# Kernel tuning notes

Hardware: AMD Instinct MI355X
Metric: run time of the kernel (lower is better)

## Reference

```python
import jax, jax.numpy as jnp
import numpy as np

B, L, D = 2, 2048, 1024
NH, KVH, DH = 16, 8, 64
GROUPS = NH // KVH
ROPE_THETA = 10000.0
SPARSITY = 0.5


def setup_inputs() -> dict:
    key = jax.random.key(0)
    ks = jax.random.split(key, 5)
    hidden_states = jax.random.normal(ks[0], (B, L, D), dtype=jnp.float32)
    wq = jax.random.normal(ks[1], (D, NH * DH), dtype=jnp.float32) * 0.02
    wk = jax.random.normal(ks[2], (D, KVH * DH), dtype=jnp.float32) * 0.02
    wv = jax.random.normal(ks[3], (D, KVH * DH), dtype=jnp.float32) * 0.02
    wo = jax.random.normal(ks[4], (NH * DH, D), dtype=jnp.float32) * 0.02
    position_ids = jnp.broadcast_to(jnp.arange(L, dtype=jnp.int64 if jax.config.jax_enable_x64 else jnp.int32), (B, L))
    return {"hidden_states": hidden_states, "wq": wq, "wk": wk, "wv": wv, "wo": wo,
            "position_ids": position_ids}


def _rope_cos_sin(position_ids, dh, theta):
    inv_freq = 1.0 / (theta ** (jnp.arange(0, dh, 2, dtype=jnp.float32) / dh))  # [dh/2]
    freqs = position_ids.astype(jnp.float32)[..., None] * inv_freq              # [B,L,dh/2]
    emb = jnp.concatenate([freqs, freqs], axis=-1)                              # [B,L,dh]
    return jnp.cos(emb)[:, None], jnp.sin(emb)[:, None]                         # [B,1,L,dh]


def _rotate_half(x):
    h = x.shape[-1] // 2
    return jnp.concatenate([-x[..., h:], x[..., :h]], axis=-1)


def _attention(hidden_states, wq, wk, wv, wo, position_ids):
    b, l, _ = hidden_states.shape
    q = (hidden_states @ wq).reshape(b, l, NH, DH).transpose(0, 2, 1, 3)    # [B,NH,L,DH]
    k = (hidden_states @ wk).reshape(b, l, KVH, DH).transpose(0, 2, 1, 3)   # [B,KVH,L,DH]
    v = (hidden_states @ wv).reshape(b, l, KVH, DH).transpose(0, 2, 1, 3)

    cos, sin = _rope_cos_sin(position_ids, DH, ROPE_THETA)
    q = q * cos + _rotate_half(q) * sin
    k = k * cos + _rotate_half(k) * sin

    # repeat_kv: expand kv heads to match query heads (interleaved like torch)
    k = jnp.repeat(k, GROUPS, axis=1)
    v = jnp.repeat(v, GROUPS, axis=1)

    scale = DH ** -0.5
    scores = jnp.einsum("bhqd,bhkd->bhqk", q, k) * scale                    # [B,NH,L,L]

    # dynamic sparsity: keep exactly top_k entries per row (scatter mask, like torch)
    top_k = max(1, int(SPARSITY * l))
    flat = scores.reshape(-1, l)                                            # [N,L]
    _, idx = jax.lax.top_k(flat, top_k)                                     # [N,k]
    rows = jnp.arange(flat.shape[0])[:, None]
    mask = jnp.zeros(flat.shape, dtype=bool).at[rows, idx].set(True)
    min_val = jnp.finfo(flat.dtype).min
    sparse = jnp.where(mask, flat, min_val).reshape(scores.shape)

    probs = jax.nn.softmax(sparse.astype(jnp.float32), axis=-1).astype(q.dtype)
    out = jnp.einsum("bhqk,bhkd->bhqd", probs, v)                            # [B,NH,L,DH]
    out = out.transpose(0, 2, 1, 3).reshape(b, l, NH * DH)
    return out @ wo


def reference(hidden_states, wq, wk, wv, wo, position_ids):
    return _attention(hidden_states, wq, wk, wv, wo, position_ids)
```

## Files before the change

kernel.cpp:

```cpp
#include <hip/hip_runtime.h>
#include <cstdint>
#include <cstddef>

typedef unsigned int u32;
typedef unsigned long long u64;
typedef __attribute__((ext_vector_type(8))) short s8v;
typedef __attribute__((ext_vector_type(4))) float f4v;
typedef __attribute__((ext_vector_type(4))) unsigned short us4;

#define B_   2
#define L_   2048
#define D_   1024
#define NH_  16
#define KVH_ 8
#define DH_  64
#define TOPK_ 1024

#define MFMA16(a, b, c) __builtin_amdgcn_mfma_f32_16x16x32_bf16(a, b, c, 0, 0, 0)

__device__ __forceinline__ u32 fkey(float s) {
    u32 b = __float_as_uint(s);
    return b ^ ((u32)((int)b >> 31) | 0x80000000u);
}
__device__ __forceinline__ float fkeyinv(u32 k) {
    u32 b = (k & 0x80000000u) ? (k ^ 0x80000000u) : ~k;
    return __uint_as_float(b);
}
__device__ __forceinline__ unsigned short bf16rne(float x) {
    u32 u = __float_as_uint(x);
    u32 r = (u + 0x7FFFu + ((u >> 16) & 1u)) >> 16;
    return (unsigned short)r;
}
__device__ __forceinline__ float bf2f(unsigned short h) {
    return __uint_as_float((u32)h << 16);
}

__global__ __launch_bounds__(256) void prep_wt_all(
    const float* __restrict__ wq, const float* __restrict__ wk,
    const float* __restrict__ wv, const float* __restrict__ wo,
    unsigned short* __restrict__ QKVWh, unsigned short* __restrict__ QKVWl,
    unsigned short* __restrict__ WoH, unsigned short* __restrict__ WoL) {
    __shared__ float tile[64 * 65];
    const int k0 = blockIdx.x * 64;
    const int byy = blockIdx.y;
    const float* W;
    unsigned short *Dh, *Dl;
    int N, n0, nrow;
    if (byy < 16)      { W = wq; N = 1024; n0 = byy * 64;        Dh = QKVWh; Dl = QKVWl; nrow = byy * 64; }
    else if (byy < 24) { W = wk; N = 512;  n0 = (byy - 16) * 64; Dh = QKVWh; Dl = QKVWl; nrow = 1024 + (byy - 16) * 64; }
    else if (byy < 32) { W = wv; N = 512;  n0 = (byy - 24) * 64; Dh = QKVWh; Dl = QKVWl; nrow = 1536 + (byy - 24) * 64; }
    else               { W = wo; N = 1024; n0 = (byy - 32) * 64; Dh = WoH;   Dl = WoL;   nrow = (byy - 32) * 64; }
    int t = threadIdx.x;
#pragma unroll
    for (int i = 0; i < 16; ++i) {
        int idx = t + i * 256;
        int kk = idx >> 6, nn = idx & 63;
        tile[kk * 65 + nn] = W[(size_t)(k0 + kk) * N + n0 + nn];
    }
    __syncthreads();
#pragma unroll
    for (int i = 0; i < 16; ++i) {
        int idx = t + i * 256;
        int nn = idx >> 6, kk = idx & 63;
        float x = tile[kk * 65 + nn];
        unsigned short hi = bf16rne(x);
        unsigned short lo = bf16rne(x - bf2f(hi));
        Dh[(size_t)(nrow + nn) * 1024 + k0 + kk] = hi;
        Dl[(size_t)(nrow + nn) * 1024 + k0 + kk] = lo;
    }
}

__global__ __launch_bounds__(256) void split_a(const float* __restrict__ A,
                                               unsigned short* __restrict__ AH,
                                               unsigned short* __restrict__ AL) {
    size_t tid = (size_t)blockIdx.x * 256 + threadIdx.x;
    float4 v = *(const float4*)(A + tid * 4);
    us4 hv, lv;
    float x[4] = {v.x, v.y, v.z, v.w};
#pragma unroll
    for (int i = 0; i < 4; ++i) {
        unsigned short hi = bf16rne(x[i]);
        hv[i] = hi;
        lv[i] = bf16rne(x[i] - bf2f(hi));
    }
    *(us4*)(AH + tid * 4) = hv;
    *(us4*)(AL + tid * 4) = lv;
}

__global__ __launch_bounds__(256) void gemm_bf(
    const unsigned short* __restrict__ Ah,
    const unsigned short* __restrict__ Al,
    int lda,
    const unsigned short* __restrict__ Wh,
    const unsigned short* __restrict__ Wl,
    float* __restrict__ C, int K, int N) {
    __shared__ __align__(16) unsigned short lAh[128 * 40];
    __shared__ __align__(16) unsigned short lAl[128 * 40];
    __shared__ __align__(16) unsigned short lBh[128 * 40];
    __shared__ __align__(16) unsigned short lBl[128 * 40];
    const int t = threadIdx.x, lane = t & 63, w = t >> 6;
    const int quad = lane >> 4, col = lane & 15;
    const int wm = w >> 1, wn = w & 1;
    const int nwg = gridDim.x * gridDim.y;
    const int lin = blockIdx.y * gridDim.x + blockIdx.x;
    const int swz = (lin & 7) * (nwg >> 3) + (lin >> 3);
    const int bx = swz % gridDim.x, by = swz / gridDim.x;
    const int m0 = bx * 128, n0 = by * 128;
    const int sr = t >> 1, sk = (t & 1) * 16;

    f4v acc[4][4];
#pragma unroll
    for (int i = 0; i < 4; ++i)
#pragma unroll
        for (int j = 0; j < 4; ++j) acc[i][j] = (f4v){0.f, 0.f, 0.f, 0.f};

    for (int k0 = 0; k0 < K; k0 += 32) {
        const unsigned short* ap = Ah + (size_t)(m0 + sr) * lda + k0 + sk;
        const unsigned short* alp = Al + (size_t)(m0 + sr) * lda + k0 + sk;
        s8v a_h0 = *(const s8v*)(ap);
        s8v a_h1 = *(const s8v*)(ap + 8);
        s8v a_l0 = *(const s8v*)(alp);
        s8v a_l1 = *(const s8v*)(alp + 8);
        s8v bh0 = *(const s8v*)(Wh + (size_t)(n0 + sr) * K + k0 + sk);
        s8v bh1 = *(const s8v*)(Wh + (size_t)(n0 + sr) * K + k0 + sk + 8);
        s8v bl0 = *(const s8v*)(Wl + (size_t)(n0 + sr) * K + k0 + sk);
        s8v bl1 = *(const s8v*)(Wl + (size_t)(n0 + sr) * K + k0 + sk + 8);
        __syncthreads();
        *(s8v*)&lAh[sr * 40 + sk]     = a_h0;
        *(s8v*)&lAh[sr * 40 + sk + 8] = a_h1;
        *(s8v*)&lAl[sr * 40 + sk]     = a_l0;
        *(s8v*)&lAl[sr * 40 + sk + 8] = a_l1;
        *(s8v*)&lBh[sr * 40 + sk]     = bh0;
        *(s8v*)&lBh[sr * 40 + sk + 8] = bh1;
        *(s8v*)&lBl[sr * 40 + sk]     = bl0;
        *(s8v*)&lBl[sr * 40 + sk + 8] = bl1;
        __syncthreads();
        s8v amh[4], aml[4], bnh[4], bnl[4];
#pragma unroll
        for (int mt = 0; mt < 4; ++mt) {
            amh[mt] = *(s8v*)&lAh[(wm * 64 + mt * 16 + col) * 40 + quad * 8];
            aml[mt] = *(s8v*)&lAl[(wm * 64 + mt * 16 + col) * 40 + quad * 8];
        }
#pragma unroll
        for (int nt = 0; nt < 4; ++nt) {
            bnh[nt] = *(s8v*)&lBh[(wn * 64 + nt * 16 + col) * 40 + quad * 8];
            bnl[nt] = *(s8v*)&lBl[(wn * 64 + nt * 16 + col) * 40 + quad * 8];
        }
#pragma unroll
        for (int mt = 0; mt < 4; ++mt)
#pragma unroll
            for (int nt = 0; nt < 4; ++nt) {
                acc[mt][nt] = MFMA16(amh[mt], bnh[nt], acc[mt][nt]);
                acc[mt][nt] = MFMA16(amh[mt], bnl[nt], acc[mt][nt]);
                acc[mt][nt] = MFMA16(aml[mt], bnh[nt], acc[mt][nt]);
            }
    }
#pragma unroll
    for (int mt = 0; mt < 4; ++mt)
#pragma unroll
        for (int nt = 0; nt < 4; ++nt)
#pragma unroll
            for (int r = 0; r < 4; ++r)
                C[(size_t)(m0 + wm * 64 + mt * 16 + quad * 4 + r) * N +
                  n0 + wn * 64 + nt * 16 + col] = acc[mt][nt][r];
}

__global__ __launch_bounds__(256) void rope_q(float* __restrict__ Q,
                                              const int* __restrict__ pos) {
    int tid = blockIdx.x * 256 + threadIdx.x;
    int dl = tid & 31;
    int h  = (tid >> 5) & 15;
    int l  = (tid >> 9) & 2047;
    int b  = tid >> 20;
    size_t base = (size_t)(b * L_ + l) * 2048 + h * DH_;
    float x1 = Q[base + dl];
    float x2 = Q[base + dl + 32];
    float p = (float)pos[b * L_ + l];
    float invf = (float)pow(10000.0, -(double)dl / 32.0);
    float a = p * invf;
    float s, c;
    sincosf(a, &s, &c);
    Q[base + dl]      = x1 * c - x2 * s;
    Q[base + dl + 32] = x2 * c + x1 * s;
}

__global__ __launch_bounds__(256) void prep_k(const float* __restrict__ QKV,
                                              unsigned short* __restrict__ KHp,
                                              unsigned short* __restrict__ KLp,
                                              const int* __restrict__ pos) {
    int tid = blockIdx.x * 256 + threadIdx.x;
    int d   = tid & 63;
    int l   = (tid >> 6) & 2047;
    int kvh = (tid >> 17) & 7;
    int b   = tid >> 20;
    size_t src = (size_t)(b * L_ + l) * 2048 + 1024 + kvh * DH_;
    float x  = QKV[src + d];
    int dp   = (d < 32) ? d + 32 : d - 32;
    float xp = QKV[src + dp];
    float p = (float)pos[b * L_ + l];
    int i = d & 31;
    float invf = (float)pow(10000.0, -(double)i / 32.0);
    float a = p * invf;
    float s, c;
    sincosf(a, &s, &c);
    float out = (d < 32) ? (x * c - xp * s) : (x * c + xp * s);
    unsigned short hi = bf16rne(out);
    unsigned short lo = bf16rne(out - bf2f(hi));
    size_t dst = ((size_t)(b * KVH_ + kvh) * L_ + l) * DH_ + d;
    KHp[dst] = hi;
    KLp[dst] = lo;
}

__global__ __launch_bounds__(256) void prep_v(const float* __restrict__ QKV,
                                              unsigned short* __restrict__ VTp) {
    __shared__ float tile[64 * 65];
    int bid = blockIdx.x;
    int lb  = bid & 31;
    int kvh = (bid >> 5) & 7;
    int b   = bid >> 8;
    int l0  = lb * 64;
    int t   = threadIdx.x;
#pragma unroll
    for (int i = 0; i < 16; ++i) {
        int idx = t + i * 256;
        int ll = idx >> 6, d = idx & 63;
        tile[ll * 65 + d] =
            QKV[(size_t)(b * L_ + l0 + ll) * 2048 + 1536 + kvh * DH_ + d];
    }
    __syncthreads();
#pragma unroll
    for (int i = 0; i < 16; ++i) {
        int idx = t + i * 256;
        int d = idx >> 6, ll = idx & 63;
        VTp[((size_t)(b * KVH_ + kvh) * DH_ + d) * L_ + l0 + ll] = bf16rne(tile[ll * 65 + d]);
    }
}

__global__ __launch_bounds__(512, 4) void attn(
    const float* __restrict__ QR,
    const unsigned short* __restrict__ KH,
    const unsigned short* __restrict__ KL,
    const unsigned short* __restrict__ VT,
    unsigned short* __restrict__ AOus) {

    extern __shared__ __align__(16) unsigned char dynsm[];
    float* Sc = (float*)dynsm;
    unsigned short* Pc = (unsigned short*)dynsm;
    u32* hist = (u32*)dynsm;
    float* qtile  = (float*)(dynsm + 66304);
    float* outred = (float*)(dynsm + 66304);

    const int t = threadIdx.x;
    const int lane = t & 63, w = t >> 6;
    const int quad = lane >> 4, col = lane & 15;
    const int bid0 = blockIdx.x;
    const int bid  = (bid0 & 7) * 512 + (bid0 >> 3);
    const int l0  = (bid & 255) * 8;
    const int kvh = (bid >> 8) & 7;
    const int b   = bid >> 11;
    const int r0 = 2 * w, r1 = 2 * w + 1;

    if (t < 256) {
        int q = t >> 4, d4 = (t & 15) * 4;
        *(float4*)&qtile[q * 68 + d4] =
            *(const float4*)(QR + (size_t)(b * L_ + l0 + (q & 7)) * 2048 +
                             (kvh * 2 + (q >> 3)) * DH_ + d4);
    }
    __syncthreads();

    union FR { s8v v; unsigned short u[8]; };
    FR ah[2], al[2];
#pragma unroll
    for (int ks = 0; ks < 2; ++ks)
#pragma unroll
        for (int i = 0; i < 8; ++i) {
            float x = qtile[col * 68 + ks * 32 + quad * 8 + i];
            unsigned short hi = bf16rne(x);
            ah[ks].u[i] = hi;
            al[ks].u[i] = bf16rne(x - bf2f(hi));
        }

    const size_t slabK = (size_t)(b * KVH_ + kvh) * L_ * DH_;
    const unsigned short* khp = KH + slabK;
    const unsigned short* klp = KL + slabK;
    u32 ukA[32], ukB[32];

#pragma unroll
    for (int half = 0; half < 2; ++half) {
        if (half) __syncthreads();
#pragma unroll
        for (int tj = 0; tj < 8; ++tj) {
            int jl = w * 128 + tj * 16;
            int j0 = half * 1024 + jl;
            const unsigned short* kh8 = khp + (size_t)(j0 + col) * 64 + quad * 8;
            const unsigned short* kl8 = klp + (size_t)(j0 + col) * 64 + quad * 8;
            s8v bh0 = *(const s8v*)(kh8);
            s8v bh1 = *(const s8v*)(kh8 + 32);
            s8v bl0 = *(const s8v*)(kl8);
            s8v bl1 = *(const s8v*)(kl8 + 32);
            f4v c = {0.f, 0.f, 0.f, 0.f};
            c = MFMA16(ah[0].v, bh0, c);
            c = MFMA16(al[0].v, bh0, c);
            c = MFMA16(ah[0].v, bl0, c);
            c = MFMA16(ah[1].v, bh1, c);
            c = MFMA16(al[1].v, bh1, c);
            c = MFMA16(ah[1].v, bl1, c);
            c = c * 0.125f;
#pragma unroll
            for (int r = 0; r < 4; ++r)
                Sc[(quad * 4 + r) * 1034 + jl + col] = c[r];
        }
        __syncthreads();
        if (half == 0) {
            outred[t] = 0.f;
            outred[t + 512] = 0.f;
            if (t < 64) outred[1024 + t] = 0.f;
        }
#pragma unroll
        for (int i2 = 0; i2 < 16; ++i2) {
            ukA[half * 16 + i2] = fkey(Sc[r0 * 1034 + i2 * 64 + lane]);
            ukB[half * 16 + i2] = fkey(Sc[r1 * 1034 + i2 * 64 + lane]);
        }
    }
    __syncthreads();

    u32* hq = &hist[w * 1024];
    const int rep = lane & 3;
    auto middle = [&](u32 (&uk)[32]) -> float {
        u32 ulo = 0xFFFFFFFFu, uhi = 0u;
#pragma unroll
        for (int i = 0; i < 32; ++i) {
            u32 u = uk[i];
            ulo = (u < ulo) ? u : ulo;
            uhi = (u > uhi) ? u : uhi;
        }
        for (int off = 1; off < 64; off <<= 1) {
            u32 ol = (u32)__shfl_xor((int)ulo, off);
            u32 oh = (u32)__shfl_xor((int)uhi, off);
            ulo = (ol < ulo) ? ol : ulo;
            uhi = (oh > uhi) ? oh : uhi;
        }
        const float mrow = fkeyinv(uhi);
        const int sh = __clz((int)((uhi - ulo) | 1u));
#pragma unroll
        for (int i = 0; i < 32; ++i) uk[i] = (uk[i] - ulo) << sh;

        u32 pf = 0u, kq = (u32)TOPK_, ng = 0u, geq = 0u;
        for (int pass = 0; pass < 4; ++pass) {
            int shift = 24 - 8 * pass;
#pragma unroll
            for (int i = 0; i < 4; ++i)
                *(uint4*)&hq[i * 256 + lane * 4] = make_uint4(0u, 0u, 0u, 0u);
            u32 pm = pass ? (0xFFFFFFFFu << (shift + 8)) : 0u;
#pragma unroll
            for (int i = 0; i < 32; ++i) {
                u32 u = uk[i];
                if ((u & pm) == pf) {
                    u32 d = (u >> shift) & 255u;
                    atomicAdd(&hq[(d & 3) * 256 + (d >> 2) * 4 + rep], 1u);
                }
            }
            u32 hb_[4];
            u32 s4 = 0u;
#pragma unroll
            for (int bb = 0; bb < 4; ++bb) {
                uint4 hv = *(const uint4*)&hq[bb * 256 + lane * 4];
                hb_[bb] = hv.x + hv.y + hv.z + hv.w;
                s4 += hb_[bb];
            }
            u32 v = s4;
            for (int off = 1; off < 64; off <<= 1) {
                u32 tmp = __shfl_down(v, off);
                if (lane + off < 64) v += tmp;
            }
            u32 g = v - s4;
            u32 mydig = 0u, myk = 0u, myng = 0u, myhb = 0u;
            bool found = false;
#pragma unroll
            for (int bb = 3; bb >= 0; --bb) {
                u32 hb = hb_[bb];
                if (hb && g < kq && kq <= g + hb) {
                    found = true;
                    mydig = (u32)(4 * lane + bb);
                    myk   = kq - g;
                    myng  = ng + g;
                    myhb  = hb;
                }
                g += hb;
            }
            u64 fm = __ballot(found);
            int src = (int)__builtin_ctzll(fm);
            pf |= ((u32)__shfl((int)mydig, src)) << shift;
            kq  = (u32)__shfl((int)myk,  src);
            ng  = (u32)__shfl((int)myng, src);
            u32 hbs = (u32)__shfl((int)myhb, src);
            if (kq == hbs) { geq = 1u; break; }
        }

        const u32 uth = pf;
        u32 selm = 0u;
        if (geq) {
#pragma unroll
            for (int i = 0; i < 32; ++i)
                if (uk[i] >= uth) selm |= 1u << i;
        } else {
            const u32 quota = (u32)TOPK_ - ng;
            u32 eqm = 0u;
#pragma unroll
            for (int i = 0; i < 32; ++i) {
                u32 u = uk[i];
                if (u > uth) selm |= 1u << i;
                else if (u == uth) eqm |= 1u << i;
            }
            u32 ec = (u32)__builtin_popcount(eqm);
            for (int off = 1; off < 64; off <<= 1) ec += __shfl_xor(ec, off);
            if (ec == quota) {
                selm |= eqm;
            } else {
                u32 base = 0;
                u64 lmask = ((u64)1 << lane) - 1;
#pragma unroll
                for (int i = 0; i < 32; ++i) {
                    u64 mm = __ballot((eqm >> i) & 1u);
                    if ((eqm >> i) & 1u) {
                        u32 rk = base + (u32)__builtin_popcountll(mm & lmask);
                        if (rk < quota) selm |= 1u << i;
                    }
                    base += (u32)__builtin_popcountll(mm);
                }
            }
        }

        float z = 0.f;
#pragma unroll
        for (int i = 0; i < 32; ++i) {
            float vv = fkeyinv((uk[i] >> sh) + ulo);
            float e = ((selm >> i) & 1u) ? __expf(vv - mrow) : 0.f;
            uk[i] = __float_as_uint(e);
            z += e;
        }
        for (int off = 1; off < 64; off <<= 1) z += __shfl_xor(z, off);
        return 1.0f / z;
    };

    float invZA = middle(ukA);
    float invZB = middle(ukB);

    const unsigned short* vt = VT + (size_t)(b * KVH_ + kvh) * DH_ * L_;
    const int jb0 = w * 256 + quad * 8;
    s8v pv0 = *(const s8v*)(vt + (size_t)( 0 + col) * L_ + jb0);
    s8v pv1 = *(const s8v*)(vt + (size_t)(16 + col) * L_ + jb0);
    s8v pv2 = *(const s8v*)(vt + (size_t)(32 + col) * L_ + jb0);
    s8v pv3 = *(const s8v*)(vt + (size_t)(48 + col) * L_ + jb0);

    __syncthreads();

#pragma unroll
    for (int i = 0; i < 32; ++i) {
        int jp = 1024 * (i >> 4) + 64 * (i & 15) + lane;
        Pc[r0 * 2072 + jp] = bf16rne(__uint_as_float(ukA[i]) * invZA);
        Pc[r1 * 2072 + jp] = bf16rne(__uint_as_float(ukB[i]) * invZB);
    }
    __syncthreads();

    f4v acc0 = {0.f, 0.f, 0.f, 0.f}, acc1 = acc0, acc2 = acc0, acc3 = acc0;
    {
        s8v ap = *(const s8v*)&Pc[col * 2072 + jb0];
        acc0 = MFMA16(ap, pv0, acc0);
        acc1 = MFMA16(ap, pv1, acc1);
        acc2 = MFMA16(ap, pv2, acc2);
        acc3 = MFMA16(ap, pv3, acc3);
    }
#pragma unroll
    for (int kc = 1; kc < 8; ++kc) {
        int jb = w * 256 + kc * 32 + quad * 8;
        s8v ap = *(const s8v*)&Pc[col * 2072 + jb];
        s8v v0 = *(const s8v*)(vt + (size_t)( 0 + col) * L_ + jb);
        s8v v1 = *(const s8v*)(vt + (size_t)(16 + col) * L_ + jb);
        s8v v2 = *(const s8v*)(vt + (size_t)(32 + col) * L_ + jb);
        s8v v3 = *(const s8v*)(vt + (size_t)(48 + col) * L_ + jb);
        acc0 = MFMA16(ap, v0, acc0);
        acc1 = MFMA16(ap, v1, acc1);
        acc2 = MFMA16(ap, v2, acc2);
        acc3 = MFMA16(ap, v3, acc3);
    }

#pragma unroll
    for (int r = 0; r < 4; ++r) {
        atomicAdd(&outred[(quad * 4 + r) * 68 +  0 + col], acc0[r]);
        atomicAdd(&outred[(quad * 4 + r) * 68 + 16 + col], acc1[r]);
        atomicAdd(&outred[(quad * 4 + r) * 68 + 32 + col], acc2[r]);
        atomicAdd(&outred[(quad * 4 + r) * 68 + 48 + col], acc3[r]);
    }
    __syncthreads();
    if (t < 256) {
        int q = t >> 4, d4 = (t & 15) * 4;
        float4 o = *(float4*)&outred[q * 68 + d4];
        size_t m = (size_t)(b * L_ + l0 + (q & 7));
        int n = (kvh * 2 + (q >> 3)) * DH_ + d4;
        float x[4] = {o.x, o.y, o.z, o.w};
        us4 hv, lv;
#pragma unroll
        for (int i = 0; i < 4; ++i) {
            unsigned short hi = bf16rne(x[i]);
            hv[i] = hi;
            lv[i] = bf16rne(x[i] - bf2f(hi));
        }
        *(us4*)(AOus + m * 4096 + 2048 + n) = hv;
        *(us4*)(AOus + m * 4096 + 3072 + n) = lv;
    }
}

extern "C" void kernel_launch(void* const* d_in, const int* in_sizes, int n_in,
                              void* d_out, int out_size, void* d_ws, size_t ws_size,
                              hipStream_t stream) {
    const float* hs = (const float*)d_in[0];
    const float* wq = (const float*)d_in[1];
    const float* wk = (const float*)d_in[2];
    const float* wv = (const float*)d_in[3];
    const float* wo = (const float*)d_in[4];
    const int*  pos = (const int*)d_in[5];

    float* ws = (float*)d_ws;
    const size_t M1 = 1u << 20;
    float* QKV = ws;
    unsigned short* QKVWh = (unsigned short*)(ws +  8 * M1);
    unsigned short* QKVWl = (unsigned short*)(ws +  9 * M1);
    unsigned short* WoH   = (unsigned short*)(ws + 10 * M1);
    unsigned short* WoL   = (unsigned short*)(ws + 10 * M1 + M1 / 2);
    unsigned short* KH    = (unsigned short*)(ws + 11 * M1);
    unsigned short* KL    = (unsigned short*)(ws + 12 * M1);
    unsigned short* VT    = (unsigned short*)(ws + 13 * M1);
    unsigned short* hsH   = (unsigned short*)(ws + 11 * M1);
    unsigned short* hsL   = (unsigned short*)(ws + 13 * M1);
    float* out = (float*)d_out;

    static bool attr_set = false;
    if (!attr_set) {
        hipFuncSetAttribute((const void*)attn,
                            hipFuncAttributeMaxDynamicSharedMemorySize, 70656);
        attr_set = true;
    }

    dim3 blk(256);
    prep_wt_all<<<dim3(16, 48), blk, 0, stream>>>(wq, wk, wv, wo,
                                                  QKVWh, QKVWl, WoH, WoL);
    split_a<<<dim3(4096), blk, 0, stream>>>(hs, hsH, hsL);
    gemm_bf<<<dim3(32, 16), blk, 0, stream>>>(hsH, hsL, 1024, QKVWh, QKVWl,
                                              QKV, 1024, 2048);
    rope_q<<<dim3(8192), blk, 0, stream>>>(QKV, pos);
    prep_k<<<dim3(8192), blk, 0, stream>>>(QKV, KH, KL, pos);
    prep_v<<<dim3(512),  blk, 0, stream>>>(QKV, VT);
    attn<<<dim3(4096), dim3(512), 70656, stream>>>(QKV, KH, KL, VT,
                                                   (unsigned short*)QKV);
    gemm_bf<<<dim3(32, 8), blk, 0, stream>>>((unsigned short*)QKV + 2048,
                                             (unsigned short*)QKV + 3072, 4096,
                                             WoH, WoL, out, 1024, 1024);
}
```

Before: 767.3 us.

## Fuse RoPE, K split and V transpose into QKV GEMM epilogue

Result: no change. 755.6 us (-1.5%).

```diff
diff --git a/kernel.cpp b/kernel.cpp
--- a/kernel.cpp
+++ b/kernel.cpp
@@ -165,74 +165,131 @@
                   n0 + wn * 64 + nt * 16 + col] = acc[mt][nt][r];
 }
 
-__global__ __launch_bounds__(256) void rope_q(float* __restrict__ Q,
-                                              const int* __restrict__ pos) {
-    int tid = blockIdx.x * 256 + threadIdx.x;
-    int dl = tid & 31;
-    int h  = (tid >> 5) & 15;
-    int l  = (tid >> 9) & 2047;
-    int b  = tid >> 20;
-    size_t base = (size_t)(b * L_ + l) * 2048 + h * DH_;
-    float x1 = Q[base + dl];
-    float x2 = Q[base + dl + 32];
-    float p = (float)pos[b * L_ + l];
-    float invf = (float)pow(10000.0, -(double)dl / 32.0);
-    float a = p * invf;
-    float s, c;
-    sincosf(a, &s, &c);
-    Q[base + dl]      = x1 * c - x2 * s;
-    Q[base + dl + 32] = x2 * c + x1 * s;
-}
-
-__global__ __launch_bounds__(256) void prep_k(const float* __restrict__ QKV,
-                                              unsigned short* __restrict__ KHp,
-                                              unsigned short* __restrict__ KLp,
-                                              const int* __restrict__ pos) {
-    int tid = blockIdx.x * 256 + threadIdx.x;
-    int d   = tid & 63;
-    int l   = (tid >> 6) & 2047;
-    int kvh = (tid >> 17) & 7;
-    int b   = tid >> 20;
-    size_t src = (size_t)(b * L_ + l) * 2048 + 1024 + kvh * DH_;
-    float x  = QKV[src + d];
-    int dp   = (d < 32) ? d + 32 : d - 32;
-    float xp = QKV[src + dp];
-    float p = (float)pos[b * L_ + l];
-    int i = d & 31;
-    float invf = (float)pow(10000.0, -(double)i / 32.0);
-    float a = p * invf;
-    float s, c;
-    sincosf(a, &s, &c);
-    float out = (d < 32) ? (x * c - xp * s) : (x * c + xp * s);
-    unsigned short hi = bf16rne(out);
-    unsigned short lo = bf16rne(out - bf2f(hi));
-    size_t dst = ((size_t)(b * KVH_ + kvh) * L_ + l) * DH_ + d;
-    KHp[dst] = hi;
-    KLp[dst] = lo;
-}
-
-__global__ __launch_bounds__(256) void prep_v(const float* __restrict__ QKV,
-                                              unsigned short* __restrict__ VTp) {
-    __shared__ float tile[64 * 65];
-    int bid = blockIdx.x;
-    int lb  = bid & 31;
-    int kvh = (bid >> 5) & 7;
-    int b   = bid >> 8;
-    int l0  = lb * 64;
-    int t   = threadIdx.x;
-#pragma unroll
-    for (int i = 0; i < 16; ++i) {
-        int idx = t + i * 256;
-        int ll = idx >> 6, d = idx & 63;
-        tile[ll * 65 + d] =
-            QKV[(size_t)(b * L_ + l0 + ll) * 2048 + 1536 + kvh * DH_ + d];
-    }
-    __syncthreads();
-#pragma unroll
-    for (int i = 0; i < 16; ++i) {
-        int idx = t + i * 256;
-        int d = idx >> 6, ll = idx & 63;
-        VTp[((size_t)(b * KVH_ + kvh) * DH_ + d) * L_ + l0 + ll] = bf16rne(tile[ll * 65 + d]);
+__global__ __launch_bounds__(256) void gemm_qkv(
+    const unsigned short* __restrict__ Ah,
+    const unsigned short* __restrict__ Al,
+    const unsigned short* __restrict__ Wh,
+    const unsigned short* __restrict__ Wl,
+    const int* __restrict__ pos,
+    float* __restrict__ Qrope,
+    unsigned short* __restrict__ KHp,
+    unsigned short* __restrict__ KLp,
+    unsigned short* __restrict__ VTp) {
+    const int K = 1024, lda = 1024;
+    __shared__ __align__(16) unsigned short lAh[128 * 40];
+    __shared__ __align__(16) unsigned short lAl[128 * 40];
+    __shared__ __align__(16) unsigned short lBh[128 * 40];
+    __shared__ __align__(16) unsigned short lBl[128 * 40];
+    const int t = threadIdx.x, lane = t & 63, w = t >> 6;
+    const int quad = lane >> 4, col = lane & 15;
+    const int wm = w >> 1, wn = w & 1;
+    const int nwg = gridDim.x * gridDim.y;
+    const int lin = blockIdx.y * gridDim.x + blockIdx.x;
+    const int swz = (lin & 7) * (nwg >> 3) + (lin >> 3);
+    const int bx = swz % gridDim.x, by = swz / gridDim.x;
+    const int m0 = bx * 128, n0 = by * 128;
+    const int sr = t >> 1, sk = (t & 1) * 16;
+
+    f4v acc[4][4];
+#pragma unroll
+    for (int i = 0; i < 4; ++i)
+#pragma unroll
+        for (int j = 0; j < 4; ++j) acc[i][j] = (f4v){0.f, 0.f, 0.f, 0.f};
+
+    for (int k0 = 0; k0 < K; k0 += 32) {
+        const unsigned short* ap = Ah + (size_t)(m0 + sr) * lda + k0 + sk;
+        const unsigned short* alp = Al + (size_t)(m0 + sr) * lda + k0 + sk;
+        s8v a_h0 = *(const s8v*)(ap);
+        s8v a_h1 = *(const s8v*)(ap + 8);
+        s8v a_l0 = *(const s8v*)(alp);
+        s8v a_l1 = *(const s8v*)(alp + 8);
+        s8v bh0 = *(const s8v*)(Wh + (size_t)(n0 + sr) * K + k0 + sk);
+        s8v bh1 = *(const s8v*)(Wh + (size_t)(n0 + sr) * K + k0 + sk + 8);
+        s8v bl0 = *(const s8v*)(Wl + (size_t)(n0 + sr) * K + k0 + sk);
+        s8v bl1 = *(const s8v*)(Wl + (size_t)(n0 + sr) * K + k0 + sk + 8);
+        __syncthreads();
+        *(s8v*)&lAh[sr * 40 + sk]     = a_h0;
+        *(s8v*)&lAh[sr * 40 + sk + 8] = a_h1;
+        *(s8v*)&lAl[sr * 40 + sk]     = a_l0;
+        *(s8v*)&lAl[sr * 40 + sk + 8] = a_l1;
+        *(s8v*)&lBh[sr * 40 + sk]     = bh0;
+        *(s8v*)&lBh[sr * 40 + sk + 8] = bh1;
+        *(s8v*)&lBl[sr * 40 + sk]     = bl0;
+        *(s8v*)&lBl[sr * 40 + sk + 8] = bl1;
+        __syncthreads();
+        s8v amh[4], aml[4], bnh[4], bnl[4];
+#pragma unroll
+        for (int mt = 0; mt < 4; ++mt) {
+            amh[mt] = *(s8v*)&lAh[(wm * 64 + mt * 16 + col) * 40 + quad * 8];
+            aml[mt] = *(s8v*)&lAl[(wm * 64 + mt * 16 + col) * 40 + quad * 8];
+        }
+#pragma unroll
+        for (int nt = 0; nt < 4; ++nt) {
+            bnh[nt] = *(s8v*)&lBh[(wn * 64 + nt * 16 + col) * 40 + quad * 8];
+            bnl[nt] = *(s8v*)&lBl[(wn * 64 + nt * 16 + col) * 40 + quad * 8];
+        }
+#pragma unroll
+        for (int mt = 0; mt < 4; ++mt)
+#pragma unroll
+            for (int nt = 0; nt < 4; ++nt) {
+                acc[mt][nt] = MFMA16(amh[mt], bnh[nt], acc[mt][nt]);
+                acc[mt][nt] = MFMA16(amh[mt], bnl[nt], acc[mt][nt]);
+                acc[mt][nt] = MFMA16(aml[mt], bnh[nt], acc[mt][nt]);
+            }
+    }
+
+    const int hb = n0 + wn * 64;
+    if (hb < 1024 + 512) {
+        float invf0 = (float)pow(10000.0, -(double)col / 32.0);
+        float invf1 = (float)pow(10000.0, -(double)(16 + col) / 32.0);
+        const int isK = (hb >= 1024);
+        const int kvh = isK ? ((hb - 1024) >> 6) : 0;
+#pragma unroll
+        for (int mt = 0; mt < 4; ++mt)
+#pragma unroll
+            for (int r = 0; r < 4; ++r) {
+                int row = m0 + wm * 64 + mt * 16 + quad * 4 + r;
+                float p = (float)pos[row];
+                float s0, c0, s1, c1;
+                sincosf(p * invf0, &s0, &c0);
+                sincosf(p * invf1, &s1, &c1);
+                float x0 = acc[mt][0][r], y0 = acc[mt][2][r];
+                float x1 = acc[mt][1][r], y1 = acc[mt][3][r];
+                float oA = x0 * c0 - y0 * s0;
+                float oB = y0 * c0 + x0 * s0;
+                float oC = x1 * c1 - y1 * s1;
+                float oD = y1 * c1 + x1 * s1;
+                if (!isK) {
+                    size_t base = (size_t)row * 1024 + hb;
+                    Qrope[base + col]      = oA;
+                    Qrope[base + col + 32] = oB;
+                    Qrope[base + col + 16] = oC;
+                    Qrope[base + col + 48] = oD;
+                } else {
+                    int b = row >> 11, l = row & 2047;
+                    size_t base = ((size_t)(b * KVH_ + kvh) * L_ + l) * DH_;
+                    unsigned short h;
+                    h = bf16rne(oA); KHp[base + col]      = h; KLp[base + col]      = bf16rne(oA - bf2f(h));
+                    h = bf16rne(oB); KHp[base + col + 32] = h; KLp[base + col + 32] = bf16rne(oB - bf2f(h));
+                    h = bf16rne(oC); KHp[base + col + 16] = h; KLp[base + col + 16] = bf16rne(oC - bf2f(h));
+                    h = bf16rne(oD); KHp[base + col + 48] = h; KLp[base + col + 48] = bf16rne(oD - bf2f(h));
+                }
+            }
+    } else {
+        const int kvh = (hb - 1536) >> 6;
+#pragma unroll
+        for (int mt = 0; mt < 4; ++mt)
+#pragma unroll
+            for (int nt = 0; nt < 4; ++nt) {
+                int d = nt * 16 + col;
+                int row0 = m0 + wm * 64 + mt * 16 + quad * 4;
+                int b = row0 >> 11, l = row0 & 2047;
+                size_t base = ((size_t)(b * KVH_ + kvh) * DH_ + d) * L_ + l;
+                us4 vv;
+#pragma unroll
+                for (int r = 0; r < 4; ++r) vv[r] = bf16rne(acc[mt][nt][r]);
+                *(us4*)(VTp + base) = vv;
+            }
     }
 }
 
@@ -263,7 +320,7 @@
     if (t < 256) {
         int q = t >> 4, d4 = (t & 15) * 4;
         *(float4*)&qtile[q * 68 + d4] =
-            *(const float4*)(QR + (size_t)(b * L_ + l0 + (q & 7)) * 2048 +
+            *(const float4*)(QR + (size_t)(b * L_ + l0 + (q & 7)) * 1024 +
                              (kvh * 2 + (q >> 3)) * DH_ + d4);
     }
     __syncthreads();
@@ -506,8 +563,8 @@
             hv[i] = hi;
             lv[i] = bf16rne(x[i] - bf2f(hi));
         }
-        *(us4*)(AOus + m * 4096 + 2048 + n) = hv;
-        *(us4*)(AOus + m * 4096 + 3072 + n) = lv;
+        *(us4*)(AOus + m * 2048 + n) = hv;
+        *(us4*)(AOus + m * 2048 + 1024 + n) = lv;
     }
 }
 
@@ -523,7 +580,10 @@
 
     float* ws = (float*)d_ws;
     const size_t M1 = 1u << 20;
-    float* QKV = ws;
+    float* Qrope = ws;
+    unsigned short* hsH  = (unsigned short*)(ws + 4 * M1);
+    unsigned short* hsL  = (unsigned short*)(ws + 6 * M1);
+    unsigned short* AOus = (unsigned short*)(ws + 4 * M1);
     unsigned short* QKVWh = (unsigned short*)(ws +  8 * M1);
     unsigned short* QKVWl = (unsigned short*)(ws +  9 * M1);
     unsigned short* WoH   = (unsigned short*)(ws + 10 * M1);
@@ -531,8 +591,6 @@
     unsigned short* KH    = (unsigned short*)(ws + 11 * M1);
     unsigned short* KL    = (unsigned short*)(ws + 12 * M1);
     unsigned short* VT    = (unsigned short*)(ws + 13 * M1);
-    unsigned short* hsH   = (unsigned short*)(ws + 11 * M1);
-    unsigned short* hsL   = (unsigned short*)(ws + 13 * M1);
     float* out = (float*)d_out;
 
     static bool attr_set = false;
@@ -546,14 +604,9 @@
     prep_wt_all<<<dim3(16, 48), blk, 0, stream>>>(wq, wk, wv, wo,
                                                   QKVWh, QKVWl, WoH, WoL);
     split_a<<<dim3(4096), blk, 0, stream>>>(hs, hsH, hsL);
-    gemm_bf<<<dim3(32, 16), blk, 0, stream>>>(hsH, hsL, 1024, QKVWh, QKVWl,
-                                              QKV, 1024, 2048);
-    rope_q<<<dim3(8192), blk, 0, stream>>>(QKV, pos);
-    prep_k<<<dim3(8192), blk, 0, stream>>>(QKV, KH, KL, pos);
-    prep_v<<<dim3(512),  blk, 0, stream>>>(QKV, VT);
-    attn<<<dim3(4096), dim3(512), 70656, stream>>>(QKV, KH, KL, VT,
-                                                   (unsigned short*)QKV);
-    gemm_bf<<<dim3(32, 8), blk, 0, stream>>>((unsigned short*)QKV + 2048,
-                                             (unsigned short*)QKV + 3072, 4096,
+    gemm_qkv<<<dim3(32, 16), blk, 0, stream>>>(hsH, hsL, QKVWh, QKVWl, pos,
+                                               Qrope, KH, KL, VT);
+    attn<<<dim3(4096), dim3(512), 70656, stream>>>(Qrope, KH, KL, VT, AOus);
+    gemm_bf<<<dim3(32, 8), blk, 0, stream>>>(AOus, AOus + 1024, 2048,
                                              WoH, WoL, out, 1024, 1024);
 }
```
